# Kernel optimization log

Measured on AMD Instinct MI355X. Metric: run time of the kernel, lower is better.

The kernel has to match this reference:

```python
import jax, jax.numpy as jnp
import numpy as np

N_QUBITS = 8
D_K = 64
B, S = 8, 1024


def _single_qubit_states(xang, theta):
    # xang: [B,S,n] values in [-1,1] (post-tanh); theta: [n,3] Rot params (phi, theta, omega)
    # state = RZ(omega) @ RY(th) @ RZ(phi) @ RY(pi*xang) |0>
    a = xang * jnp.pi
    c = jnp.cos(a * 0.5)          # [B,S,n]
    s = jnp.sin(a * 0.5)
    phi, th, om = theta[:, 0], theta[:, 1], theta[:, 2]   # each [n]
    ct = jnp.cos(th * 0.5)
    st = jnp.sin(th * 0.5)
    e_mpo = jnp.exp(-0.5j * (phi + om))   # e^{-i(phi+omega)/2}
    e_pmo = jnp.exp(0.5j * (phi - om))    # e^{+i(phi-omega)/2}
    amp0 = e_mpo * ct * c - e_pmo * st * s
    amp1 = jnp.conj(e_pmo) * st * c + jnp.conj(e_mpo) * ct * s
    return jnp.stack([amp0, amp1], axis=-1)   # [B,S,n,2] complex64


def setup_inputs() -> dict:
    key = jax.random.key(0)
    k1, k2, k3, k4 = jax.random.split(key, 4)
    x = jax.random.normal(k1, (B, S, D_K), dtype=jnp.float32)
    theta_q = jax.random.normal(k2, (N_QUBITS, 3), dtype=jnp.float32) * 0.1
    theta_k = jax.random.normal(k3, (N_QUBITS, 3), dtype=jnp.float32) * 0.1
    W_v = jax.random.normal(k4, (D_K, D_K), dtype=jnp.float32) / np.sqrt(D_K)
    b_v = jnp.zeros((D_K,), dtype=jnp.float32)
    return {"x": x, "theta_q": theta_q, "theta_k": theta_k, "W_v": W_v, "b_v": b_v}


def reference(x, theta_q, theta_k, W_v, b_v):
    n = theta_q.shape[0]
    xn = jnp.tanh(x[..., :n])                 # [B,S,n]
    qs = _single_qubit_states(xn, theta_q)    # [B,S,n,2]
    ks = _single_qubit_states(xn, theta_k)    # [B,S,n,2]
    # per-qubit overlap <q_i | k_j> for every (b, s, t) pair
    ov = jnp.einsum('bsnc,btnc->bstn', jnp.conj(qs), ks)  # [B,S,S,n] complex
    mag2 = jnp.real(ov) ** 2 + jnp.imag(ov) ** 2
    core = jnp.prod(mag2, axis=-1)            # |<psi_q|psi_k>|^2 = swap-test <Z>
    scores = (core + 1.0) * 0.5               # [B,S,S]
    attn = jax.nn.softmax(scores, axis=-1)
    values = x @ W_v.T + b_v                  # [B,S,D]
    out = jnp.einsum('bst,btd->bsd', attn, values)
    return out, attn
```

## Files before the change

kernel.cpp:

```cpp
#include <hip/hip_runtime.h>
#include <hip/hip_fp16.h>
#include <math.h>

#define NQ 8
#define DK 64
#define NB 8
#define NS 1024
#define RB 4
#define EPITCH 1032

typedef _Float16 h2v __attribute__((ext_vector_type(2)));

__device__ __forceinline__ float fdot2h(unsigned qu, unsigned ku, float acc) {
#if defined(__has_builtin) && __has_builtin(__builtin_amdgcn_fdot2)
    union { unsigned u; h2v h; } a, b;
    a.u = qu; b.u = ku;
    return __builtin_amdgcn_fdot2(a.h, b.h, acc, false);
#else
    __half2 qh = *(__half2*)&qu, kh = *(__half2*)&ku;
    float2 qf = __half22float2(qh), kf = __half22float2(kh);
    return fmaf(qf.x, kf.x, fmaf(qf.y, kf.y, acc));
#endif
}

__global__ __launch_bounds__(256) void prep_kernel(
    const float* __restrict__ x,
    const float* __restrict__ theta_q,
    const float* __restrict__ theta_k,
    const float* __restrict__ Wv,
    const float* __restrict__ bv,
    __half* __restrict__ qdh, __half* __restrict__ kdh,
    __half* __restrict__ v2) {
    int bid = blockIdx.x;
    int tid = threadIdx.x;
    if (bid < 2048) {
        int t = bid * 4 + (tid >> 6);
        int d = tid & 63;
        const float4* xr = (const float4*)(x + (size_t)t * DK);
        const float4* wr = (const float4*)(Wv + (size_t)d * DK);
        float a0 = bv[d], a1 = 0.f, a2 = 0.f, a3 = 0.f;
#pragma unroll
        for (int j = 0; j < DK / 4; ++j) {
            float4 xv = xr[j], wv = wr[j];
            a0 = fmaf(xv.x, wv.x, a0);
            a1 = fmaf(xv.y, wv.y, a1);
            a2 = fmaf(xv.z, wv.z, a2);
            a3 = fmaf(xv.w, wv.w, a3);
        }
        float v = (a0 + a1) + (a2 + a3);
        int b = t >> 10, ti = t & 1023;
        v2[((size_t)(b * 512 + (ti >> 1)) * 64 + d) * 2 + (ti & 1)] = __float2half_rn(v);
    } else {
        __shared__ float tt[2][NQ][6];
        if (tid < 16) {
            int side = tid >> 3, n = tid & 7;
            const float* thp = side ? theta_k : theta_q;
            float phi = thp[n * 3 + 0], th = thp[n * 3 + 1], om = thp[n * 3 + 2];
            float st, ct; __sincosf(0.5f * th, &st, &ct);
            float smpo, cmpo; __sincosf(0.5f * (phi + om), &smpo, &cmpo);
            float spmo, cpmo; __sincosf(0.5f * (phi - om), &spmo, &cpmo);
            tt[side][n][0] = ct;  tt[side][n][1] = st;
            tt[side][n][2] = cmpo; tt[side][n][3] = smpo;
            tt[side][n][4] = cpmo; tt[side][n][5] = spmo;
        }
        __syncthreads();

        int gid = (bid - 2048) * 256 + tid;
        int tok = gid >> 3;
        int n = gid & 7;
        float xin = x[(size_t)tok * DK + n];
        float ex = __expf(2.0f * xin);
        float xn = 1.0f - 2.0f / (ex + 1.0f);
        float s, c;
        __sincosf(xn * 1.57079632679489662f, &s, &c);

#pragma unroll
        for (int side = 0; side < 2; ++side) {
            float ct = tt[side][n][0], st = tt[side][n][1];
            float cmpo = tt[side][n][2], smpo = tt[side][n][3];
            float cpmo = tt[side][n][4], spmo = tt[side][n][5];
            float a = ct * c, b2 = st * s, cc = st * c, d2 = ct * s;
            float a0re =  cmpo * a - cpmo * b2;
            float a0im = -smpo * a - spmo * b2;
            float a1re =  cpmo * cc + cmpo * d2;
            float a1im = -spmo * cc + smpo * d2;
            float d0 = fmaf(a0re, a0re, a0im * a0im);
            float d1 = fmaf(a1re, a1re, a1im * a1im);
            float ur = fmaf(a1re, a0re, a1im * a0im);
            float ui = fmaf(a1im, a0re, -a1re * a0im);
            if (side == 0) {
                __half2* qp = (__half2*)(qdh + (size_t)tok * 32 + n * 4);
                qp[0] = __floats2half2_rn(d0, d1);
                qp[1] = __floats2half2_rn(ur, ui);
            } else {
                __half2* kp = (__half2*)(kdh + (size_t)tok * 32 + n * 4);
                kp[0] = __floats2half2_rn(d0, d1);
                kp[1] = __floats2half2_rn(2.f * ur, 2.f * ui);
            }
        }
    }
}

__global__ __launch_bounds__(256, 4) void attn_kernel(
    const __half* __restrict__ qdh, const __half* __restrict__ kdh,
    const __half* __restrict__ v2,
    float* __restrict__ out, float* __restrict__ attn) {
    __shared__ __align__(16) unsigned char smem[16 * RB * 64 * 4];
    __half (*e16)[EPITCH] = (__half(*)[EPITCH])smem;
    float* red = (float*)smem;
    __shared__ float red_lds[4][RB];
    __shared__ float inv_lds[RB];

    int tid = threadIdx.x;
    int gr0 = blockIdx.x * RB;
    int b = gr0 >> 10;
    int w = tid >> 6, lane = tid & 63;

    const __half* kfb = kdh + (size_t)b * NS * 32;

    unsigned sq[RB][16];
#pragma unroll
    for (int r = 0; r < RB; ++r) {
        const unsigned* qp = (const unsigned*)(qdh + (size_t)(gr0 + r) * 32);
#pragma unroll
        for (int i = 0; i < 16; ++i) sq[r][i] = __builtin_amdgcn_readfirstlane(qp[i]);
    }

    float sums[RB];
#pragma unroll
    for (int r = 0; r < RB; ++r) sums[r] = 0.f;

    int t0 = w * 256;
#pragma unroll
    for (int j = 0; j < 4; ++j) {
        int t = t0 + j * 64 + lane;
        const uint4* kp = (const uint4*)(kfb + (size_t)t * 32);
        uint4 k0 = kp[0], k1 = kp[1], k2 = kp[2], k3 = kp[3];
#pragma unroll
        for (int r = 0; r < RB; ++r) {
            float m0 = fdot2h(sq[r][ 0], k0.x, fdot2h(sq[r][ 1], k0.y, 0.f));
            float m1 = fdot2h(sq[r][ 2], k0.z, fdot2h(sq[r][ 3], k0.w, 0.f));
            float m2 = fdot2h(sq[r][ 4], k1.x, fdot2h(sq[r][ 5], k1.y, 0.f));
            float m3 = fdot2h(sq[r][ 6], k1.z, fdot2h(sq[r][ 7], k1.w, 0.f));
            float m4 = fdot2h(sq[r][ 8], k2.x, fdot2h(sq[r][ 9], k2.y, 0.f));
            float m5 = fdot2h(sq[r][10], k2.z, fdot2h(sq[r][11], k2.w, 0.f));
            float m6 = fdot2h(sq[r][12], k3.x, fdot2h(sq[r][13], k3.y, 0.f));
            float m7 = fdot2h(sq[r][14], k3.z, fdot2h(sq[r][15], k3.w, 0.f));
            float core = ((m0 * m1) * (m2 * m3)) * ((m4 * m5) * (m6 * m7));
            float e = __expf(fmaf(core, 0.5f, 0.5f));
            e16[r][t] = __float2half_rn(e);
            sums[r] += e;
        }
    }

#pragma unroll
    for (int r = 0; r < RB; ++r) {
#pragma unroll
        for (int m = 1; m < 64; m <<= 1) sums[r] += __shfl_xor(sums[r], m, 64);
    }
    if (lane == 0) {
#pragma unroll
        for (int r = 0; r < RB; ++r) red_lds[w][r] = sums[r];
    }
    __syncthreads();
    if (tid < RB)
        inv_lds[tid] = 1.f / (red_lds[0][tid] + red_lds[1][tid] + red_lds[2][tid] + red_lds[3][tid]);
    __syncthreads();

    float* ab = attn + (size_t)gr0 * NS;
#pragma unroll
    for (int r = 0; r < RB; ++r) {
        float iv = inv_lds[r];
        uint2 raw = *(const uint2*)&e16[r][tid * 4];
        __half2* hp = (__half2*)&raw;
        float2 lo = __half22float2(hp[0]), hi = __half22float2(hp[1]);
        *(float4*)&ab[(size_t)r * NS + tid * 4] =
            make_float4(lo.x * iv, lo.y * iv, hi.x * iv, hi.y * iv);
    }

    int tg = tid >> 4, dg = tid & 15;
    const __half* v2b = v2 + (size_t)b * 512 * 128;
    float acc[RB][4];
#pragma unroll
    for (int r = 0; r < RB; ++r) { acc[r][0] = acc[r][1] = acc[r][2] = acc[r][3] = 0.f; }

    for (int jj = 0; jj < 32; ++jj) {
        int p = jj * 16 + tg;
        uint4 vv = *(const uint4*)(v2b + (size_t)p * 128 + dg * 8);
        unsigned ep[RB];
#pragma unroll
        for (int r = 0; r < RB; ++r) ep[r] = *(const unsigned*)&e16[r][2 * p];
#pragma unroll
        for (int r = 0; r < RB; ++r) {
            acc[r][0] = fdot2h(ep[r], vv.x, acc[r][0]);
            acc[r][1] = fdot2h(ep[r], vv.y, acc[r][1]);
            acc[r][2] = fdot2h(ep[r], vv.z, acc[r][2]);
            acc[r][3] = fdot2h(ep[r], vv.w, acc[r][3]);
        }
    }

    __syncthreads();
#pragma unroll
    for (int r = 0; r < RB; ++r) {
        *(float4*)&red[((size_t)tg * RB + r) * 64 + dg * 4] =
            make_float4(acc[r][0], acc[r][1], acc[r][2], acc[r][3]);
    }
    __syncthreads();
    {
        int r2 = tid >> 6, d = tid & 63;
        float o = 0.f;
#pragma unroll
        for (int g = 0; g < 16; ++g) o += red[((size_t)g * RB + r2) * 64 + d];
        out[((size_t)(gr0 + r2)) * DK + d] = o * inv_lds[r2];
    }
}

extern "C" void kernel_launch(void* const* d_in, const int* in_sizes, int n_in,
                              void* d_out, int out_size, void* d_ws, size_t ws_size,
                              hipStream_t stream) {
    const float* x       = (const float*)d_in[0];
    const float* theta_q = (const float*)d_in[1];
    const float* theta_k = (const float*)d_in[2];
    const float* W_v     = (const float*)d_in[3];
    const float* b_v     = (const float*)d_in[4];

    float* out  = (float*)d_out;
    float* attn = (float*)d_out + (size_t)NB * NS * DK;

    __half* qdh = (__half*)d_ws;
    __half* kdh = qdh + (size_t)NB * NS * 32;
    __half* v2  = kdh + (size_t)NB * NS * 32;

    prep_kernel<<<2048 + NB * NS * NQ / 256, 256, 0, stream>>>(
        x, theta_q, theta_k, W_v, b_v, qdh, kdh, v2);
    attn_kernel<<<NB * NS / RB, 256, 0, stream>>>(qdh, kdh, v2, out, attn);
}
```

Baseline: 51.50 us.

## Process eight query rows per block with register-cached key tiles

Doubles the rows per block from 4 to 8, so each K and V load is reused across twice as many query rows and half as many blocks are launched. The K tile is loaded once into registers and the row loop is moved to the outside, with the query coefficients read per row. The shared buffer is resized to hold eight exp rows, and the output reduction now runs in two halves of four rows to fit the existing scratch area. This raises register pressure and may reduce occupancy under the 4-waves launch bound, and the grid of 1024 blocks may underfill the device.

Result: no change. 52.37 us (+1.7%).

```diff
diff --git a/kernel.cpp b/kernel.cpp
--- a/kernel.cpp
+++ b/kernel.cpp
@@ -6,7 +6,7 @@
 #define DK 64
 #define NB 8
 #define NS 1024
-#define RB 4
+#define RB 8
 #define EPITCH 1032
 
 typedef _Float16 h2v __attribute__((ext_vector_type(2)));
@@ -105,7 +105,7 @@
     const __half* __restrict__ qdh, const __half* __restrict__ kdh,
     const __half* __restrict__ v2,
     float* __restrict__ out, float* __restrict__ attn) {
-    __shared__ __align__(16) unsigned char smem[16 * RB * 64 * 4];
+    __shared__ __align__(16) unsigned char smem[RB * EPITCH * 2];
     __half (*e16)[EPITCH] = (__half(*)[EPITCH])smem;
     float* red = (float*)smem;
     __shared__ float red_lds[4][RB];
@@ -118,37 +118,37 @@
 
     const __half* kfb = kdh + (size_t)b * NS * 32;
 
-    unsigned sq[RB][16];
+    int t0 = w * 256;
+    uint4 kv[4][4];
+#pragma unroll
+    for (int j = 0; j < 4; ++j) {
+        const uint4* kp = (const uint4*)(kfb + (size_t)(t0 + j * 64 + lane) * 32);
+        kv[j][0] = kp[0]; kv[j][1] = kp[1]; kv[j][2] = kp[2]; kv[j][3] = kp[3];
+    }
+
+    float sums[RB];
+#pragma unroll
+    for (int r = 0; r < RB; ++r) sums[r] = 0.f;
+
 #pragma unroll
     for (int r = 0; r < RB; ++r) {
         const unsigned* qp = (const unsigned*)(qdh + (size_t)(gr0 + r) * 32);
-#pragma unroll
-        for (int i = 0; i < 16; ++i) sq[r][i] = __builtin_amdgcn_readfirstlane(qp[i]);
-    }
-
-    float sums[RB];
-#pragma unroll
-    for (int r = 0; r < RB; ++r) sums[r] = 0.f;
-
-    int t0 = w * 256;
-#pragma unroll
-    for (int j = 0; j < 4; ++j) {
-        int t = t0 + j * 64 + lane;
-        const uint4* kp = (const uint4*)(kfb + (size_t)t * 32);
-        uint4 k0 = kp[0], k1 = kp[1], k2 = kp[2], k3 = kp[3];
-#pragma unroll
-        for (int r = 0; r < RB; ++r) {
-            float m0 = fdot2h(sq[r][ 0], k0.x, fdot2h(sq[r][ 1], k0.y, 0.f));
-            float m1 = fdot2h(sq[r][ 2], k0.z, fdot2h(sq[r][ 3], k0.w, 0.f));
-            float m2 = fdot2h(sq[r][ 4], k1.x, fdot2h(sq[r][ 5], k1.y, 0.f));
-            float m3 = fdot2h(sq[r][ 6], k1.z, fdot2h(sq[r][ 7], k1.w, 0.f));
-            float m4 = fdot2h(sq[r][ 8], k2.x, fdot2h(sq[r][ 9], k2.y, 0.f));
-            float m5 = fdot2h(sq[r][10], k2.z, fdot2h(sq[r][11], k2.w, 0.f));
-            float m6 = fdot2h(sq[r][12], k3.x, fdot2h(sq[r][13], k3.y, 0.f));
-            float m7 = fdot2h(sq[r][14], k3.z, fdot2h(sq[r][15], k3.w, 0.f));
+        unsigned sq[16];
+#pragma unroll
+        for (int i = 0; i < 16; ++i) sq[i] = __builtin_amdgcn_readfirstlane(qp[i]);
+#pragma unroll
+        for (int j = 0; j < 4; ++j) {
+            float m0 = fdot2h(sq[ 0], kv[j][0].x, fdot2h(sq[ 1], kv[j][0].y, 0.f));
+            float m1 = fdot2h(sq[ 2], kv[j][0].z, fdot2h(sq[ 3], kv[j][0].w, 0.f));
+            float m2 = fdot2h(sq[ 4], kv[j][1].x, fdot2h(sq[ 5], kv[j][1].y, 0.f));
+            float m3 = fdot2h(sq[ 6], kv[j][1].z, fdot2h(sq[ 7], kv[j][1].w, 0.f));
+            float m4 = fdot2h(sq[ 8], kv[j][2].x, fdot2h(sq[ 9], kv[j][2].y, 0.f));
+            float m5 = fdot2h(sq[10], kv[j][2].z, fdot2h(sq[11], kv[j][2].w, 0.f));
+            float m6 = fdot2h(sq[12], kv[j][3].x, fdot2h(sq[13], kv[j][3].y, 0.f));
+            float m7 = fdot2h(sq[14], kv[j][3].z, fdot2h(sq[15], kv[j][3].w, 0.f));
             float core = ((m0 * m1) * (m2 * m3)) * ((m4 * m5) * (m6 * m7));
             float e = __expf(fmaf(core, 0.5f, 0.5f));
-            e16[r][t] = __float2half_rn(e);
+            e16[r][t0 + j * 64 + lane] = __float2half_rn(e);
             sums[r] += e;
         }
     }
@@ -199,19 +199,21 @@
         }
     }
 
-    __syncthreads();
-#pragma unroll
-    for (int r = 0; r < RB; ++r) {
-        *(float4*)&red[((size_t)tg * RB + r) * 64 + dg * 4] =
-            make_float4(acc[r][0], acc[r][1], acc[r][2], acc[r][3]);
-    }
-    __syncthreads();
-    {
+#pragma unroll
+    for (int h = 0; h < 2; ++h) {
+        __syncthreads();
+#pragma unroll
+        for (int r = 0; r < 4; ++r) {
+            *(float4*)&red[((size_t)tg * 4 + r) * 64 + dg * 4] =
+                make_float4(acc[h * 4 + r][0], acc[h * 4 + r][1],
+                            acc[h * 4 + r][2], acc[h * 4 + r][3]);
+        }
+        __syncthreads();
         int r2 = tid >> 6, d = tid & 63;
         float o = 0.f;
 #pragma unroll
-        for (int g = 0; g < 16; ++g) o += red[((size_t)g * RB + r2) * 64 + d];
-        out[((size_t)(gr0 + r2)) * DK + d] = o * inv_lds[r2];
+        for (int g = 0; g < 16; ++g) o += red[((size_t)g * 4 + r2) * 64 + d];
+        out[((size_t)(gr0 + h * 4 + r2)) * DK + d] = o * inv_lds[h * 4 + r2];
     }
 }
 
```
